# Kernel tuning notes

Hardware: AMD Instinct MI355X
Metric: run time of the kernel (lower is better)

The kernel has to match this reference:

```python
import jax, jax.numpy as jnp
import numpy as np

N_NODES = 50000
N_EDGES = 600000
D = 128
LN_EPS = 1e-5


def setup_inputs() -> dict:
    key = jax.random.key(0)
    ks = jax.random.split(key, 10)
    s = 1.0 / np.sqrt(D)
    return {
        "node_reps": jax.random.normal(ks[0], (N_NODES, D), jnp.float32),
        "edge_reps": jax.random.normal(ks[1], (N_EDGES, D), jnp.float32),
        "src_idx": jax.random.randint(ks[2], (N_EDGES,), 0, N_NODES, jnp.int32),
        "dst_idx": jnp.sort(jax.random.randint(ks[3], (N_EDGES,), 0, N_NODES, jnp.int32)),
        "Wq": jax.random.normal(ks[4], (D, D), jnp.float32) * s,
        "Wk": jax.random.normal(ks[5], (D, D), jnp.float32) * s,
        "Wv": jax.random.normal(ks[6], (D, D), jnp.float32) * s,
        "Wo": jax.random.normal(ks[7], (D, D), jnp.float32) * s,
        "ln_gamma": jnp.ones((D,), jnp.float32),
        "ln_beta": jnp.zeros((D,), jnp.float32),
        "W1": jax.random.normal(ks[8], (3 * D, D), jnp.float32) * (1.0 / np.sqrt(3 * D)),
        "b1": jnp.zeros((D,), jnp.float32),
        "W2": jax.random.normal(ks[9], (D, D), jnp.float32) * s,
        "b2": jnp.zeros((D,), jnp.float32),
    }


def _layer_norm(x, g, b):
    mu = jnp.mean(x, axis=-1, keepdims=True)
    var = jnp.mean(jnp.square(x - mu), axis=-1, keepdims=True)
    return (x - mu) * jax.lax.rsqrt(var + LN_EPS) * g + b


def reference(node_reps, edge_reps, src_idx, dst_idx, Wq, Wk, Wv, Wo,
              ln_gamma, ln_beta, W1, b1, W2, b2):
    n_nodes, d = node_reps.shape
    # dense projections once per node (kernel-friendly GEMMs)
    q = node_reps @ Wq                                  # [N, d]
    k_nodes = node_reps @ Wk                            # [N, d]
    v_nodes = node_reps @ Wv                            # [N, d]
    # per-edge gather + edge bias
    k_e = k_nodes[src_idx] + edge_reps                  # [E, d]
    scores = jnp.sum(q[dst_idx] * k_e, axis=-1) / jnp.sqrt(jnp.float32(d))  # [E]
    # segment softmax over edges sharing the same dst node
    seg_max = jax.ops.segment_max(scores, dst_idx, num_segments=n_nodes)
    ex = jnp.exp(scores - seg_max[dst_idx])
    denom = jax.ops.segment_sum(ex, dst_idx, num_segments=n_nodes)
    alpha = ex / denom[dst_idx]                          # [E]
    v_e = v_nodes[src_idx] + edge_reps                   # [E, d]
    agg = jax.ops.segment_sum(alpha[:, None] * v_e, dst_idx, num_segments=n_nodes)  # [N, d]
    updated = _layer_norm(node_reps + agg @ Wo, ln_gamma, ln_beta)  # [N, d]
    # triplet fusion MLP over (dst node, edge, src node)
    h_trip = jnp.concatenate([node_reps[dst_idx], edge_reps, node_reps[src_idx]], axis=-1)  # [E, 3d]
    fused = jax.nn.relu(h_trip @ W1 + b1) @ W2 + b2      # [E, d]
    return updated, fused
```

## Files before the change

### kernel.cpp

```cpp
#include <hip/hip_runtime.h>
#include <hip/hip_bf16.h>

#define NN 50000
#define NE 600000
#define D 128

typedef __bf16 bf16x8 __attribute__((ext_vector_type(8)));
typedef __bf16 bf16x4 __attribute__((ext_vector_type(4)));
typedef float f32x4 __attribute__((ext_vector_type(4)));


static __device__ __forceinline__ void gload_lds16(const void* g, void* l) {
  __builtin_amdgcn_global_load_lds(
      (const __attribute__((address_space(1))) unsigned int*)g,
      (__attribute__((address_space(3))) unsigned int*)l, 16, 0, 0);
}

static __device__ __forceinline__ bf16x8 load_a_frag_nc(const float* __restrict__ A,
                                                        int row, int k0) {
  const f32x4* p = (const f32x4*)(A + (size_t)row * D + k0);
  f32x4 v0 = p[0], v1 = p[1];
  bf16x8 r;
  r[0] = (__bf16)v0[0]; r[1] = (__bf16)v0[1]; r[2] = (__bf16)v0[2]; r[3] = (__bf16)v0[3];
  r[4] = (__bf16)v1[0]; r[5] = (__bf16)v1[1]; r[6] = (__bf16)v1[2]; r[7] = (__bf16)v1[3];
  return r;
}

static __device__ __forceinline__ void stage_a_tile64(const float* __restrict__ A, int M,
                                                      int row_base, char* lds, int tid) {
  const int l32 = tid & 31;
  const int g = tid >> 5;
#pragma unroll
  for (int it = 0; it < 8; ++it) {
    int rl = it * 8 + g;
    int r = row_base + rl;
    f32x4 v = {};
    if (r < M) v = *(const f32x4*)(A + (size_t)r * D + l32 * 4);
    bf16x4 b;
    b[0] = (__bf16)v[0]; b[1] = (__bf16)v[1]; b[2] = (__bf16)v[2]; b[3] = (__bf16)v[3];
    int byte = (rl * 256 + l32 * 8) ^ ((rl & 7) << 4);
    *(bf16x4*)(lds + byte) = b;
  }
}

static __device__ __forceinline__ bf16x8 read_a_frag(const char* lds, int rl, int k0) {
  int byte = (rl * 256 + k0 * 2) ^ ((rl & 7) << 4);
  return *(const bf16x8*)(lds + byte);
}

template <int CTRL>
static __device__ __forceinline__ float dpp_add(float x) {
  int v = __builtin_amdgcn_update_dpp(0, __float_as_int(x), CTRL, 0xf, 0xf, true);
  return x + __int_as_float(v);
}

static __device__ __forceinline__ float red32(float x) {
  x = dpp_add<0xB1>(x);
  x = dpp_add<0x4E>(x);
  x = dpp_add<0x124>(x);
  x = dpp_add<0x128>(x);
  return x + __shfl_xor(x, 16, 64);
}

struct PrepArgs {
  const float* W[8];
  __bf16* WT[8];
  const int* dst;
  int* offs;
};

__global__ void prep_all(PrepArgs pa) {
  int b = blockIdx.x;
  if (b < 512) {
    int w = b >> 6;
    int t = (b & 63) * 256 + threadIdx.x;
    int n = t & 127, k = t >> 7;
    pa.WT[w][n * 128 + k] = (__bf16)pa.W[w][k * 128 + n];
  } else {
    int n = (b - 512) * 256 + threadIdx.x;
    if (n > NN) return;
    int lo = 0, hi = NE;
    while (lo < hi) {
      int mid = (lo + hi) >> 1;
      if (pa.dst[mid] < n) lo = mid + 1; else hi = mid;
    }
    pa.offs[n] = lo;
  }
}

struct GemmBatch {
  const __bf16* BT[5];
  void* C[5];
  const float* bias[5];
  int mode[5];
};

__global__ __launch_bounds__(256) void gemm_k128_b(const float* __restrict__ A,
                                                   GemmBatch gb, int M) {
  __shared__ __align__(16) char atile[64 * 256];
  const int tid = threadIdx.x;
  const int lane = tid & 63;
  const int wave = tid >> 6;
  const int wr = wave >> 1, wc = wave & 1;
  const int row0 = blockIdx.x * 64;
  const int col0 = wc * 64;
  const int lr = lane & 15;
  const int lk = (lane >> 4) << 3;
  const int rr = (lane >> 4) * 4;

  stage_a_tile64(A, M, row0, atile, tid);
  __syncthreads();

#pragma unroll
  for (int y = 0; y < 5; ++y) {
    const __bf16* __restrict__ BT = gb.BT[y];
    f32x4 acc[2][4] = {};
#pragma unroll
    for (int kk = 0; kk < 4; ++kk) {
      const int k0 = kk * 32 + lk;
      bf16x8 a[2], b[4];
#pragma unroll
      for (int m = 0; m < 2; ++m) a[m] = read_a_frag(atile, wr * 32 + m * 16 + lr, k0);
#pragma unroll
      for (int n = 0; n < 4; ++n) b[n] = *(const bf16x8*)(BT + (size_t)(col0 + n * 16 + lr) * D + k0);
#pragma unroll
      for (int m = 0; m < 2; ++m)
#pragma unroll
        for (int n = 0; n < 4; ++n)
          acc[m][n] = __builtin_amdgcn_mfma_f32_16x16x32_bf16(a[m], b[n], acc[m][n], 0, 0, 0);
    }
    float bv[4] = {0.f, 0.f, 0.f, 0.f};
    if (gb.bias[y]) {
#pragma unroll
      for (int n = 0; n < 4; ++n) bv[n] = gb.bias[y][col0 + n * 16 + lr];
    }
    const int mode = gb.mode[y];
#pragma unroll
    for (int m = 0; m < 2; ++m)
#pragma unroll
      for (int j = 0; j < 4; ++j) {
        const int r = row0 + wr * 32 + m * 16 + rr + j;
        if (r < M) {
#pragma unroll
          for (int n = 0; n < 4; ++n) {
            const int c = col0 + n * 16 + lr;
            const float val = acc[m][n][j] + bv[n];
            if (mode == 0) {
              ((float*)gb.C[y])[(size_t)r * D + c] = val;
            } else if (mode == 1) {
              ((__bf16*)gb.C[y])[(size_t)r * D + c] = (__bf16)val;
            } else if (mode == 2) {
              ((__bf16*)gb.C[y])[(size_t)r * 256 + c] = (__bf16)val;
            } else {
              ((__bf16*)gb.C[y])[(size_t)r * 256 + 128 + c] = (__bf16)val;
            }
          }
        }
      }
  }
}

#define LD1(P, K, J, SV)                                                     \
  do {                                                                       \
    const int jj_ = (J);                                                     \
    const int jc_ = jj_ < jm ? jj_ : 0;                                      \
    int si_ = __shfl((SV), jj_ & 31, 32);                                    \
    si_ = jj_ < jm ? si_ : 0;                                                \
    kb##P[K] = *(const bf16x4*)(KV + (size_t)si_ * 256 + (l32 << 2));        \
    vb##P[K] = *(const bf16x4*)(KV + (size_t)si_ * 256 + 128 + (l32 << 2));  \
    eb##P[K] = *(const f32x4*)(edge + (size_t)(s0 + jc_) * D + (l32 << 2));  \
  } while (0)

#define LOADC(P, C)                                                          \
  do {                                                                       \
    const int c4_ = (C) * 4;                                                 \
    const int sv_ = (c4_ < 32) ? sidx0 : sidx1;                              \
    LD1(P, 0, c4_ + 0, sv_); LD1(P, 1, c4_ + 1, sv_);                        \
    LD1(P, 2, c4_ + 2, sv_); LD1(P, 3, c4_ + 3, sv_);                        \
  } while (0)

#define CP1(P, K, J)                                                         \
  do {                                                                       \
    const int jj_ = (J);                                                     \
    f32x4 ef_ = eb##P[K];                                                    \
    float x0_ = (float)kb##P[K][0] + ef_[0];                                 \
    float x1_ = (float)kb##P[K][1] + ef_[1];                                 \
    float x2_ = (float)kb##P[K][2] + ef_[2];                                 \
    float x3_ = (float)kb##P[K][3] + ef_[3];                                 \
    float pp_ = fmaf(qs[1], x1_, qs[0] * x0_) + fmaf(qs[3], x3_, qs[2] * x2_); \
    float s_ = red32(pp_);                                                   \
    float w_ = jj_ < jm ? exp2f(s_) : 0.f;                                   \
    l += w_;                                                                 \
    a[0] = fmaf(w_, (float)vb##P[K][0] + ef_[0], a[0]);                      \
    a[1] = fmaf(w_, (float)vb##P[K][1] + ef_[1], a[1]);                      \
    a[2] = fmaf(w_, (float)vb##P[K][2] + ef_[2], a[2]);                      \
    a[3] = fmaf(w_, (float)vb##P[K][3] + ef_[3], a[3]);                      \
  } while (0)

#define COMPC(P, C)                                                          \
  do {                                                                       \
    const int cc4_ = (C) * 4;                                                \
    CP1(P, 0, cc4_ + 0); CP1(P, 1, cc4_ + 1);                                \
    CP1(P, 2, cc4_ + 2); CP1(P, 3, cc4_ + 3);                                \
  } while (0)

__global__ __launch_bounds__(256) __attribute__((amdgpu_waves_per_eu(3)))
void fused_edge_attn(
    const float* __restrict__ edge,
    const __bf16* __restrict__ W1bT,
    const __bf16* __restrict__ W2T,
    const __bf16* __restrict__ P1,
    const __bf16* __restrict__ P3,
    const int* __restrict__ dst,
    const int* __restrict__ src,
    const float* __restrict__ b2,
    float* __restrict__ out_fused,
    const float* __restrict__ Q,
    const __bf16* __restrict__ KV,
    const int* __restrict__ offs,
    const __bf16* __restrict__ WoT,
    const float* __restrict__ noderep,
    const float* __restrict__ gamma,
    const float* __restrict__ beta,
    float* __restrict__ out_updated) {
  __shared__ __align__(16) char bufA[64 * 256];
  __shared__ __align__(16) char bufB[64 * 256];
  const int tid = threadIdx.x;
  const int grp = blockIdx.x / 5;
  const int role = blockIdx.x % 5;

  if (role >= 2) {
    const int ebi = grp * 3 + (role - 2);
    const int eb = ebi * 64;
    const int lane = tid & 63;
    const int wave = tid >> 6;
    const int wr = wave >> 1, wc = wave & 1;
    const int lr = lane & 15;
    const int lk = (lane >> 4) << 3;
    const int col0 = wc * 64;

    {
      const int gr = lane >> 4;
      const int slot = lane & 15;
      int di[4], sg[4];
#pragma unroll
      for (int c = 0; c < 4; ++c) {
        int rl = wave * 16 + c * 4 + gr;
        di[c] = dst[eb + rl];
        sg[c] = src[eb + rl];
      }
#pragma unroll
      for (int c = 0; c < 4; ++c) {
        int rl = wave * 16 + c * 4 + gr;
        int sb = (slot * 16) ^ ((rl & 7) << 4);
        gload_lds16((const char*)(P1 + (size_t)di[c] * D) + sb,
                    bufA + (wave * 16 + c * 4) * 256);
        gload_lds16((const char*)(P3 + (size_t)sg[c] * D) + sb,
                    bufB + (wave * 16 + c * 4) * 256);
      }
    }

    f32x4 acc[2][4] = {};
#pragma unroll
    for (int kk = 0; kk < 4; ++kk) {
      const int k0 = kk * 32 + lk;
      bf16x8 a[2], b[4];
#pragma unroll
      for (int m = 0; m < 2; ++m) a[m] = load_a_frag_nc(edge, eb + wr * 32 + m * 16 + lr, k0);
#pragma unroll
      for (int n = 0; n < 4; ++n) b[n] = *(const bf16x8*)(W1bT + (size_t)(col0 + n * 16 + lr) * D + k0);
#pragma unroll
      for (int m = 0; m < 2; ++m)
#pragma unroll
        for (int n = 0; n < 4; ++n)
          acc[m][n] = __builtin_amdgcn_mfma_f32_16x16x32_bf16(a[m], b[n], acc[m][n], 0, 0, 0);
    }
    __syncthreads();

    const int rr = (lane >> 4) * 4;
#pragma unroll
    for (int m = 0; m < 2; ++m) {
#pragma unroll
      for (int j = 0; j < 4; ++j) {
        int rl = wr * 32 + m * 16 + rr + j;
#pragma unroll
        for (int n = 0; n < 4; ++n) {
          int c = col0 + n * 16 + lr;
          int byte = (rl * 256 + c * 2) ^ ((rl & 7) << 4);
          float g1 = (float)*(const __bf16*)(bufA + byte);
          float g3 = (float)*(const __bf16*)(bufB + byte);
          float v = fmaxf(acc[m][n][j] + g1 + g3, 0.f);
          *(__bf16*)(bufA + byte) = (__bf16)v;
        }
      }
    }
    __syncthreads();

    float b2v[4];
#pragma unroll
    for (int n = 0; n < 4; ++n) b2v[n] = b2[col0 + n * 16 + lr];
    f32x4 acc2[2][4] = {};
#pragma unroll
    for (int kk = 0; kk < 4; ++kk) {
      const int k0 = kk * 32 + lk;
      bf16x8 a[2], b[4];
#pragma unroll
      for (int m = 0; m < 2; ++m) a[m] = read_a_frag(bufA, wr * 32 + m * 16 + lr, k0);
#pragma unroll
      for (int n = 0; n < 4; ++n) b[n] = *(const bf16x8*)(W2T + (size_t)(col0 + n * 16 + lr) * D + k0);
#pragma unroll
      for (int m = 0; m < 2; ++m)
#pragma unroll
        for (int n = 0; n < 4; ++n)
          acc2[m][n] = __builtin_amdgcn_mfma_f32_16x16x32_bf16(a[m], b[n], acc2[m][n], 0, 0, 0);
    }
#pragma unroll
    for (int m = 0; m < 2; ++m)
#pragma unroll
      for (int j = 0; j < 4; ++j) {
        int rl = wr * 32 + m * 16 + rr + j;
        int e = eb + rl;
#pragma unroll
        for (int n = 0; n < 4; ++n) {
          int c = col0 + n * 16 + lr;
          out_fused[(size_t)e * D + c] = acc2[m][n][j] + b2v[n];
        }
      }
  } else {
    const int nw = tid >> 5;
    const int node = (grp * 2 + role) * 8 + nw;
    const int l32 = tid & 31;
    int s0 = offs[node], s1 = offs[node + 1];
    int cnt = s1 - s0;
    f32x4 q = *(const f32x4*)(Q + (size_t)node * D + l32 * 4);
    f32x4 qs;
    qs[0] = q[0] * 0.12751744f; qs[1] = q[1] * 0.12751744f;
    qs[2] = q[2] * 0.12751744f; qs[3] = q[3] * 0.12751744f;
    float l = 0.f;
    f32x4 a = {0.f, 0.f, 0.f, 0.f};

    const int jm = cnt < 64 ? cnt : 64;
    if (jm > 0) {
      int sidx0 = 0, sidx1 = 0;
      if (l32 < cnt) sidx0 = src[s0 + l32];
      if (l32 + 32 < cnt) sidx1 = src[s0 + 32 + l32];
      bf16x4 kb0[4], vb0[4]; f32x4 eb0[4];
      bf16x4 kb1[4], vb1[4]; f32x4 eb1[4];
      const int nch = (jm + 3) >> 2;
      LOADC(0, 0);
      for (int c = 0; c < nch; c += 2) {
        if (c + 1 < nch) LOADC(1, c + 1);
        COMPC(0, c);
        if (c + 2 < nch) LOADC(0, c + 2);
        if (c + 1 < nch) COMPC(1, c + 1);
      }
      for (int i = 64; i < cnt; ++i) {
        int si = src[s0 + i];
        bf16x4 kbx = *(const bf16x4*)(KV + (size_t)si * 256 + (l32 << 2));
        bf16x4 vbx = *(const bf16x4*)(KV + (size_t)si * 256 + 128 + (l32 << 2));
        f32x4 ef = *(const f32x4*)(edge + (size_t)(s0 + i) * D + (l32 << 2));
        float x0 = (float)kbx[0] + ef[0], x1 = (float)kbx[1] + ef[1];
        float x2 = (float)kbx[2] + ef[2], x3 = (float)kbx[3] + ef[3];
        float pp = fmaf(qs[1], x1, qs[0] * x0) + fmaf(qs[3], x3, qs[2] * x2);
        float w = exp2f(red32(pp));
        l += w;
        a[0] = fmaf(w, (float)vbx[0] + ef[0], a[0]);
        a[1] = fmaf(w, (float)vbx[1] + ef[1], a[1]);
        a[2] = fmaf(w, (float)vbx[2] + ef[2], a[2]);
        a[3] = fmaf(w, (float)vbx[3] + ef[3], a[3]);
      }
    }
    float inv = l > 0.f ? 1.f / l : 0.f;
    f32x4 r;
    r[0] = a[0] * inv; r[1] = a[1] * inv; r[2] = a[2] * inv; r[3] = a[3] * inv;

    {
      bf16x4 rb;
      rb[0] = (__bf16)r[0]; rb[1] = (__bf16)r[1];
      rb[2] = (__bf16)r[2]; rb[3] = (__bf16)r[3];
      int byte = (nw * 256 + l32 * 8) ^ ((nw & 7) << 4);
      *(bf16x4*)(bufA + byte) = rb;
    }
    __syncthreads();

    {
      const int wave = tid >> 6;
      const int lane = tid & 63;
      const int lr = lane & 15;
      const int lk = (lane >> 4) << 3;
      f32x4 acc[2] = {};
#pragma unroll
      for (int kk = 0; kk < 4; ++kk) {
        int k0 = kk * 32 + lk;
        bf16x8 af = read_a_frag(bufA, lr, k0);
#pragma unroll
        for (int t = 0; t < 2; ++t) {
          int n = wave * 2 + t;
          bf16x8 b = *(const bf16x8*)(WoT + (size_t)(n * 16 + lr) * D + k0);
          acc[t] = __builtin_amdgcn_mfma_f32_16x16x32_bf16(af, b, acc[t], 0, 0, 0);
        }
      }
      float* xl = (float*)bufB;
      const int rr = (lane >> 4) * 4;
      if (rr < 8) {
#pragma unroll
        for (int t = 0; t < 2; ++t) {
          int n = wave * 2 + t;
#pragma unroll
          for (int j = 0; j < 4; ++j)
            xl[(rr + j) * 128 + n * 16 + lr] = acc[t][j];
        }
      }
    }
    __syncthreads();

    {
      const float* xl = (const float*)bufB;
      f32x4 xv = *(const f32x4*)(xl + nw * 128 + l32 * 4);
      f32x4 nv = *(const f32x4*)(noderep + (size_t)node * D + l32 * 4);
      float x0 = xv[0] + nv[0], x1 = xv[1] + nv[1];
      float x2 = xv[2] + nv[2], x3 = xv[3] + nv[3];
      float s = red32(x0 + x1 + x2 + x3);
      float mu = s * (1.f / 128.f);
      float d0 = x0 - mu, d1 = x1 - mu, d2 = x2 - mu, d3 = x3 - mu;
      float vv = red32(d0 * d0 + d1 * d1 + d2 * d2 + d3 * d3);
      float rstd = rsqrtf(vv * (1.f / 128.f) + 1e-5f);
      f32x4 g = *(const f32x4*)(gamma + l32 * 4);
      f32x4 bb = *(const f32x4*)(beta + l32 * 4);
      f32x4 o;
      o[0] = d0 * rstd * g[0] + bb[0];
      o[1] = d1 * rstd * g[1] + bb[1];
      o[2] = d2 * rstd * g[2] + bb[2];
      o[3] = d3 * rstd * g[3] + bb[3];
      *(f32x4*)(out_updated + (size_t)node * D + l32 * 4) = o;
    }
  }
}

extern "C" void kernel_launch(void* const* d_in, const int* in_sizes, int n_in,
                              void* d_out, int out_size, void* d_ws, size_t ws_size,
                              hipStream_t stream) {
  const float* node = (const float*)d_in[0];
  const float* edge = (const float*)d_in[1];
  const int* src = (const int*)d_in[2];
  const int* dst = (const int*)d_in[3];
  const float* Wq = (const float*)d_in[4];
  const float* Wk = (const float*)d_in[5];
  const float* Wv = (const float*)d_in[6];
  const float* Wo = (const float*)d_in[7];
  const float* gamma = (const float*)d_in[8];
  const float* beta = (const float*)d_in[9];
  const float* W1 = (const float*)d_in[10];
  const float* b1 = (const float*)d_in[11];
  const float* W2 = (const float*)d_in[12];
  const float* b2 = (const float*)d_in[13];

  float* out_updated = (float*)d_out;
  float* out_fused = (float*)d_out + (size_t)NN * D;

  char* ws = (char*)d_ws;
  size_t o = 0;
  auto take = [&](size_t bytes) {
    char* p = ws + o;
    o = (o + bytes + 255) & ~(size_t)255;
    return p;
  };
  int* offs = (int*)take((NN + 1) * sizeof(int));
  __bf16* WqT = (__bf16*)take(128 * 128 * 2);
  __bf16* WkT = (__bf16*)take(128 * 128 * 2);
  __bf16* WvT = (__bf16*)take(128 * 128 * 2);
  __bf16* WoT = (__bf16*)take(128 * 128 * 2);
  __bf16* W1aT = (__bf16*)take(128 * 128 * 2);
  __bf16* W1bT = (__bf16*)take(128 * 128 * 2);
  __bf16* W1cT = (__bf16*)take(128 * 128 * 2);
  __bf16* W2T = (__bf16*)take(128 * 128 * 2);
  float* Qb = (float*)take((size_t)NN * D * 4);
  __bf16* KVb = (__bf16*)take((size_t)NN * 256 * 2);
  __bf16* P1b = (__bf16*)take((size_t)NN * D * 2);
  __bf16* P3b = (__bf16*)take((size_t)NN * D * 2);

  PrepArgs pa;
  pa.W[0] = Wq; pa.WT[0] = WqT;
  pa.W[1] = Wk; pa.WT[1] = WkT;
  pa.W[2] = Wv; pa.WT[2] = WvT;
  pa.W[3] = Wo; pa.WT[3] = WoT;
  pa.W[4] = W1; pa.WT[4] = W1aT;
  pa.W[5] = W1 + 128 * 128; pa.WT[5] = W1bT;
  pa.W[6] = W1 + 256 * 128; pa.WT[6] = W1cT;
  pa.W[7] = W2; pa.WT[7] = W2T;
  pa.dst = dst; pa.offs = offs;
  prep_all<<<512 + (NN + 256) / 256, 256, 0, stream>>>(pa);

  GemmBatch gb;
  gb.BT[0] = WqT;  gb.C[0] = Qb;  gb.bias[0] = nullptr; gb.mode[0] = 0;
  gb.BT[1] = WkT;  gb.C[1] = KVb; gb.bias[1] = nullptr; gb.mode[1] = 2;
  gb.BT[2] = WvT;  gb.C[2] = KVb; gb.bias[2] = nullptr; gb.mode[2] = 3;
  gb.BT[3] = W1aT; gb.C[3] = P1b; gb.bias[3] = b1;      gb.mode[3] = 1;
  gb.BT[4] = W1cT; gb.C[4] = P3b; gb.bias[4] = nullptr; gb.mode[4] = 1;
  gemm_k128_b<<<(NN + 63) / 64, 256, 0, stream>>>(node, gb, NN);

  fused_edge_attn<<<15625, 256, 0, stream>>>(edge, W1bT, W2T, P1b, P3b, dst, src,
                                             b2, out_fused, Qb, KVb, offs,
                                             WoT, node, gamma, beta, out_updated);
}
```

Measured before the change: 437.3 us.

## Balance attention edges across waves and split node GEMM over weight grid

Measured after the change: 437.7 us. Within noise of the previous version (+0.1%).

```diff
diff --git a/kernel.cpp b/kernel.cpp
--- a/kernel.cpp
+++ b/kernel.cpp
@@ -26,12 +26,12 @@
   return r;
 }
 
-static __device__ __forceinline__ void stage_a_tile64(const float* __restrict__ A, int M,
-                                                      int row_base, char* lds, int tid) {
+static __device__ __forceinline__ void stage_a_tile128(const float* __restrict__ A, int M,
+                                                       int row_base, char* lds, int tid) {
   const int l32 = tid & 31;
   const int g = tid >> 5;
 #pragma unroll
-  for (int it = 0; it < 8; ++it) {
+  for (int it = 0; it < 16; ++it) {
     int rl = it * 8 + g;
     int r = row_base + rl;
     f32x4 v = {};
@@ -97,99 +97,104 @@
 
 __global__ __launch_bounds__(256) void gemm_k128_b(const float* __restrict__ A,
                                                    GemmBatch gb, int M) {
-  __shared__ __align__(16) char atile[64 * 256];
+  __shared__ __align__(16) char atile[128 * 256];
+  const int y = blockIdx.y;
+  const __bf16* __restrict__ BT = gb.BT[y];
   const int tid = threadIdx.x;
   const int lane = tid & 63;
   const int wave = tid >> 6;
   const int wr = wave >> 1, wc = wave & 1;
-  const int row0 = blockIdx.x * 64;
+  const int row0 = blockIdx.x * 128;
   const int col0 = wc * 64;
   const int lr = lane & 15;
   const int lk = (lane >> 4) << 3;
+
+  stage_a_tile128(A, M, row0, atile, tid);
+  __syncthreads();
+
+  f32x4 acc[4][4] = {};
+#pragma unroll
+  for (int kk = 0; kk < 4; ++kk) {
+    const int k0 = kk * 32 + lk;
+    bf16x8 a[4], b[4];
+#pragma unroll
+    for (int m = 0; m < 4; ++m) a[m] = read_a_frag(atile, wr * 64 + m * 16 + lr, k0);
+#pragma unroll
+    for (int n = 0; n < 4; ++n) b[n] = *(const bf16x8*)(BT + (size_t)(col0 + n * 16 + lr) * D + k0);
+#pragma unroll
+    for (int m = 0; m < 4; ++m)
+#pragma unroll
+      for (int n = 0; n < 4; ++n)
+        acc[m][n] = __builtin_amdgcn_mfma_f32_16x16x32_bf16(a[m], b[n], acc[m][n], 0, 0, 0);
+  }
   const int rr = (lane >> 4) * 4;
-
-  stage_a_tile64(A, M, row0, atile, tid);
-  __syncthreads();
-
-#pragma unroll
-  for (int y = 0; y < 5; ++y) {
-    const __bf16* __restrict__ BT = gb.BT[y];
-    f32x4 acc[2][4] = {};
-#pragma unroll
-    for (int kk = 0; kk < 4; ++kk) {
-      const int k0 = kk * 32 + lk;
-      bf16x8 a[2], b[4];
-#pragma unroll
-      for (int m = 0; m < 2; ++m) a[m] = read_a_frag(atile, wr * 32 + m * 16 + lr, k0);
-#pragma unroll
-      for (int n = 0; n < 4; ++n) b[n] = *(const bf16x8*)(BT + (size_t)(col0 + n * 16 + lr) * D + k0);
-#pragma unroll
-      for (int m = 0; m < 2; ++m)
-#pragma unroll
-        for (int n = 0; n < 4; ++n)
-          acc[m][n] = __builtin_amdgcn_mfma_f32_16x16x32_bf16(a[m], b[n], acc[m][n], 0, 0, 0);
-    }
-    float bv[4] = {0.f, 0.f, 0.f, 0.f};
-    if (gb.bias[y]) {
-#pragma unroll
-      for (int n = 0; n < 4; ++n) bv[n] = gb.bias[y][col0 + n * 16 + lr];
-    }
-    const int mode = gb.mode[y];
-#pragma unroll
-    for (int m = 0; m < 2; ++m)
-#pragma unroll
-      for (int j = 0; j < 4; ++j) {
-        const int r = row0 + wr * 32 + m * 16 + rr + j;
-        if (r < M) {
-#pragma unroll
-          for (int n = 0; n < 4; ++n) {
-            const int c = col0 + n * 16 + lr;
-            const float val = acc[m][n][j] + bv[n];
-            if (mode == 0) {
-              ((float*)gb.C[y])[(size_t)r * D + c] = val;
-            } else if (mode == 1) {
-              ((__bf16*)gb.C[y])[(size_t)r * D + c] = (__bf16)val;
-            } else if (mode == 2) {
-              ((__bf16*)gb.C[y])[(size_t)r * 256 + c] = (__bf16)val;
-            } else {
-              ((__bf16*)gb.C[y])[(size_t)r * 256 + 128 + c] = (__bf16)val;
-            }
+  float bv[4] = {0.f, 0.f, 0.f, 0.f};
+  if (gb.bias[y]) {
+#pragma unroll
+    for (int n = 0; n < 4; ++n) bv[n] = gb.bias[y][col0 + n * 16 + lr];
+  }
+  const int mode = gb.mode[y];
+#pragma unroll
+  for (int m = 0; m < 4; ++m)
+#pragma unroll
+    for (int j = 0; j < 4; ++j) {
+      const int r = row0 + wr * 64 + m * 16 + rr + j;
+      if (r < M) {
+#pragma unroll
+        for (int n = 0; n < 4; ++n) {
+          const int c = col0 + n * 16 + lr;
+          const float val = acc[m][n][j] + bv[n];
+          if (mode == 0) {
+            ((float*)gb.C[y])[(size_t)r * D + c] = val;
+          } else if (mode == 1) {
+            ((__bf16*)gb.C[y])[(size_t)r * D + c] = (__bf16)val;
+          } else if (mode == 2) {
+            ((__bf16*)gb.C[y])[(size_t)r * 256 + c] = (__bf16)val;
+          } else {
+            ((__bf16*)gb.C[y])[(size_t)r * 256 + 128 + c] = (__bf16)val;
           }
         }
       }
-  }
-}
-
-#define LD1(P, K, J, SV)                                                     \
+    }
+}
+
+#define ALD1(P, K, JJ)                                                       \
   do {                                                                       \
-    const int jj_ = (J);                                                     \
-    const int jc_ = jj_ < jm ? jj_ : 0;                                      \
-    int si_ = __shfl((SV), jj_ & 31, 32);                                    \
-    si_ = jj_ < jm ? si_ : 0;                                                \
+    const int jj_ = (JJ);                                                    \
+    const int ok_ = jj_ < n32;                                               \
+    int si_ = __shfl(sidx, jj_ & 31, 32);                                    \
+    si_ = ok_ ? si_ : 0;                                                     \
+    const int ej_ = ok_ ? (myS + jj_) : myS;                                 \
     kb##P[K] = *(const bf16x4*)(KV + (size_t)si_ * 256 + (l32 << 2));        \
     vb##P[K] = *(const bf16x4*)(KV + (size_t)si_ * 256 + 128 + (l32 << 2));  \
-    eb##P[K] = *(const f32x4*)(edge + (size_t)(s0 + jc_) * D + (l32 << 2));  \
+    eb##P[K] = *(const f32x4*)(edge + (size_t)ej_ * D + (l32 << 2));         \
   } while (0)
 
-#define LOADC(P, C)                                                          \
+#define ALOADC(P, C)                                                         \
   do {                                                                       \
     const int c4_ = (C) * 4;                                                 \
-    const int sv_ = (c4_ < 32) ? sidx0 : sidx1;                              \
-    LD1(P, 0, c4_ + 0, sv_); LD1(P, 1, c4_ + 1, sv_);                        \
-    LD1(P, 2, c4_ + 2, sv_); LD1(P, 3, c4_ + 3, sv_);                        \
+    ALD1(P, 0, c4_ + 0); ALD1(P, 1, c4_ + 1);                                \
+    ALD1(P, 2, c4_ + 2); ALD1(P, 3, c4_ + 3);                                \
   } while (0)
 
-#define CP1(P, K, J)                                                         \
+#define ACP1(P, K, JJ)                                                       \
   do {                                                                       \
-    const int jj_ = (J);                                                     \
+    const int jj_ = (JJ);                                                    \
+    const int ok_ = jj_ < n32;                                               \
+    int dj_ = __shfl(didx, jj_ & 31, 32);                                    \
+    dj_ = ok_ ? dj_ : cur;                                                   \
+    if (dj_ != cur) {                                                        \
+      flush();                                                               \
+      cur = dj_;                                                             \
+      qs = *(const f32x4*)(qlds + ((cur - n0) << 7) + (l32 << 2));           \
+    }                                                                        \
     f32x4 ef_ = eb##P[K];                                                    \
     float x0_ = (float)kb##P[K][0] + ef_[0];                                 \
     float x1_ = (float)kb##P[K][1] + ef_[1];                                 \
     float x2_ = (float)kb##P[K][2] + ef_[2];                                 \
     float x3_ = (float)kb##P[K][3] + ef_[3];                                 \
     float pp_ = fmaf(qs[1], x1_, qs[0] * x0_) + fmaf(qs[3], x3_, qs[2] * x2_); \
-    float s_ = red32(pp_);                                                   \
-    float w_ = jj_ < jm ? exp2f(s_) : 0.f;                                   \
+    float w_ = ok_ ? exp2f(red32(pp_)) : 0.f;                                \
     l += w_;                                                                 \
     a[0] = fmaf(w_, (float)vb##P[K][0] + ef_[0], a[0]);                      \
     a[1] = fmaf(w_, (float)vb##P[K][1] + ef_[1], a[1]);                      \
@@ -197,12 +202,14 @@
     a[3] = fmaf(w_, (float)vb##P[K][3] + ef_[3], a[3]);                      \
   } while (0)
 
-#define COMPC(P, C)                                                          \
+#define ACOMPC(P, C)                                                         \
   do {                                                                       \
-    const int cc4_ = (C) * 4;                                                \
-    CP1(P, 0, cc4_ + 0); CP1(P, 1, cc4_ + 1);                                \
-    CP1(P, 2, cc4_ + 2); CP1(P, 3, cc4_ + 3);                                \
+    const int c4_ = (C) * 4;                                                 \
+    ACP1(P, 0, c4_ + 0); ACP1(P, 1, c4_ + 1);                                \
+    ACP1(P, 2, c4_ + 2); ACP1(P, 3, c4_ + 3);                                \
   } while (0)
+
+#define CATT 0.12751744612764933f
 
 __global__ __launch_bounds__(256) __attribute__((amdgpu_waves_per_eu(3)))
 void fused_edge_attn(
@@ -328,37 +335,71 @@
       }
   } else {
     const int nw = tid >> 5;
-    const int node = (grp * 2 + role) * 8 + nw;
     const int l32 = tid & 31;
-    int s0 = offs[node], s1 = offs[node + 1];
-    int cnt = s1 - s0;
-    f32x4 q = *(const f32x4*)(Q + (size_t)node * D + l32 * 4);
-    f32x4 qs;
-    qs[0] = q[0] * 0.12751744f; qs[1] = q[1] * 0.12751744f;
-    qs[2] = q[2] * 0.12751744f; qs[3] = q[3] * 0.12751744f;
-    float l = 0.f;
-    f32x4 a = {0.f, 0.f, 0.f, 0.f};
-
-    const int jm = cnt < 64 ? cnt : 64;
-    if (jm > 0) {
-      int sidx0 = 0, sidx1 = 0;
-      if (l32 < cnt) sidx0 = src[s0 + l32];
-      if (l32 + 32 < cnt) sidx1 = src[s0 + 32 + l32];
+    const int n0 = (grp * 2 + role) * 8;
+    float* qlds = (float*)bufA;
+    float* nodeAcc = (float*)bufB;
+
+    {
+      f32x4 qv = *(const f32x4*)(Q + (size_t)(n0 + nw) * D + (l32 << 2));
+      f32x4 qsc;
+      qsc[0] = qv[0] * CATT; qsc[1] = qv[1] * CATT;
+      qsc[2] = qv[2] * CATT; qsc[3] = qv[3] * CATT;
+      *(f32x4*)(qlds + nw * 128 + (l32 << 2)) = qsc;
+      for (int i = tid; i < 8 * 132; i += 256) nodeAcc[i] = 0.f;
+    }
+    __syncthreads();
+
+    const int e0 = offs[n0], e1 = offs[n0 + 8];
+    const int L = e1 - e0;
+    const int per = (L + 7) >> 3;
+    const int myS = e0 + nw * per;
+    const int myE = (myS + per < e1) ? (myS + per) : e1;
+    const int n = myE - myS;
+
+    if (n > 0) {
+      const int n32 = n < 32 ? n : 32;
+      int sidx = 0, didx = 0;
+      {
+        int gi = myS + l32;
+        if (l32 < n) { sidx = src[gi]; didx = dst[gi]; }
+      }
+      int cur = __shfl(didx, 0, 32);
+      f32x4 qs = *(const f32x4*)(qlds + ((cur - n0) << 7) + (l32 << 2));
+      float l = 0.f;
+      f32x4 a = {0.f, 0.f, 0.f, 0.f};
+      auto flush = [&]() {
+        float* na = nodeAcc + (cur - n0) * 132;
+        atomicAdd(na + (l32 << 2) + 0, a[0]);
+        atomicAdd(na + (l32 << 2) + 1, a[1]);
+        atomicAdd(na + (l32 << 2) + 2, a[2]);
+        atomicAdd(na + (l32 << 2) + 3, a[3]);
+        if (l32 == 0) atomicAdd(na + 128, l);
+        a[0] = 0.f; a[1] = 0.f; a[2] = 0.f; a[3] = 0.f;
+        l = 0.f;
+      };
+
       bf16x4 kb0[4], vb0[4]; f32x4 eb0[4];
       bf16x4 kb1[4], vb1[4]; f32x4 eb1[4];
-      const int nch = (jm + 3) >> 2;
-      LOADC(0, 0);
+      const int nch = (n32 + 3) >> 2;
+      ALOADC(0, 0);
       for (int c = 0; c < nch; c += 2) {
-        if (c + 1 < nch) LOADC(1, c + 1);
-        COMPC(0, c);
-        if (c + 2 < nch) LOADC(0, c + 2);
-        if (c + 1 < nch) COMPC(1, c + 1);
-      }
-      for (int i = 64; i < cnt; ++i) {
-        int si = src[s0 + i];
+        if (c + 1 < nch) ALOADC(1, c + 1);
+        ACOMPC(0, c);
+        if (c + 2 < nch) ALOADC(0, c + 2);
+        if (c + 1 < nch) ACOMPC(1, c + 1);
+      }
+      for (int i = myS + 32; i < myE; ++i) {
+        int si = src[i];
+        int dj = dst[i];
+        if (dj != cur) {
+          flush();
+          cur = dj;
+          qs = *(const f32x4*)(qlds + ((cur - n0) << 7) + (l32 << 2));
+        }
         bf16x4 kbx = *(const bf16x4*)(KV + (size_t)si * 256 + (l32 << 2));
         bf16x4 vbx = *(const bf16x4*)(KV + (size_t)si * 256 + 128 + (l32 << 2));
-        f32x4 ef = *(const f32x4*)(edge + (size_t)(s0 + i) * D + (l32 << 2));
+        f32x4 ef = *(const f32x4*)(edge + (size_t)i * D + (l32 << 2));
         float x0 = (float)kbx[0] + ef[0], x1 = (float)kbx[1] + ef[1];
         float x2 = (float)kbx[2] + ef[2], x3 = (float)kbx[3] + ef[3];
         float pp = fmaf(qs[1], x1, qs[0] * x0) + fmaf(qs[3], x3, qs[2] * x2);
@@ -369,15 +410,17 @@
         a[2] = fmaf(w, (float)vbx[2] + ef[2], a[2]);
         a[3] = fmaf(w, (float)vbx[3] + ef[3], a[3]);
       }
-    }
-    float inv = l > 0.f ? 1.f / l : 0.f;
-    f32x4 r;
-    r[0] = a[0] * inv; r[1] = a[1] * inv; r[2] = a[2] * inv; r[3] = a[3] * inv;
+      flush();
+    }
+    __syncthreads();
 
     {
+      float lsum = nodeAcc[nw * 132 + 128];
+      f32x4 av = *(const f32x4*)(nodeAcc + nw * 132 + (l32 << 2));
+      float inv = lsum > 0.f ? 1.f / lsum : 0.f;
       bf16x4 rb;
-      rb[0] = (__bf16)r[0]; rb[1] = (__bf16)r[1];
-      rb[2] = (__bf16)r[2]; rb[3] = (__bf16)r[3];
+      rb[0] = (__bf16)(av[0] * inv); rb[1] = (__bf16)(av[1] * inv);
+      rb[2] = (__bf16)(av[2] * inv); rb[3] = (__bf16)(av[3] * inv);
       int byte = (nw * 256 + l32 * 8) ^ ((nw & 7) << 4);
       *(bf16x4*)(bufA + byte) = rb;
     }
@@ -395,8 +438,8 @@
         bf16x8 af = read_a_frag(bufA, lr, k0);
 #pragma unroll
         for (int t = 0; t < 2; ++t) {
-          int n = wave * 2 + t;
-          bf16x8 b = *(const bf16x8*)(WoT + (size_t)(n * 16 + lr) * D + k0);
+          int nn = wave * 2 + t;
+          bf16x8 b = *(const bf16x8*)(WoT + (size_t)(nn * 16 + lr) * D + k0);
           acc[t] = __builtin_amdgcn_mfma_f32_16x16x32_bf16(af, b, acc[t], 0, 0, 0);
         }
       }
@@ -405,16 +448,17 @@
       if (rr < 8) {
 #pragma unroll
         for (int t = 0; t < 2; ++t) {
-          int n = wave * 2 + t;
+          int nn = wave * 2 + t;
 #pragma unroll
           for (int j = 0; j < 4; ++j)
-            xl[(rr + j) * 128 + n * 16 + lr] = acc[t][j];
+            xl[(rr + j) * 128 + nn * 16 + lr] = acc[t][j];
         }
       }
     }
     __syncthreads();
 
     {
+      const int node = n0 + nw;
       const float* xl = (const float*)bufB;
       f32x4 xv = *(const f32x4*)(xl + nw * 128 + l32 * 4);
       f32x4 nv = *(const f32x4*)(noderep + (size_t)node * D + l32 * 4);
@@ -491,13 +535,14 @@
   pa.dst = dst; pa.offs = offs;
   prep_all<<<512 + (NN + 256) / 256, 256, 0, stream>>>(pa);
 
+  int gnode = (NN + 127) / 128;
   GemmBatch gb;
   gb.BT[0] = WqT;  gb.C[0] = Qb;  gb.bias[0] = nullptr; gb.mode[0] = 0;
   gb.BT[1] = WkT;  gb.C[1] = KVb; gb.bias[1] = nullptr; gb.mode[1] = 2;
   gb.BT[2] = WvT;  gb.C[2] = KVb; gb.bias[2] = nullptr; gb.mode[2] = 3;
   gb.BT[3] = W1aT; gb.C[3] = P1b; gb.bias[3] = b1;      gb.mode[3] = 1;
   gb.BT[4] = W1cT; gb.C[4] = P3b; gb.bias[4] = nullptr; gb.mode[4] = 1;
-  gemm_k128_b<<<(NN + 63) / 64, 256, 0, stream>>>(node, gb, NN);
+  gemm_k128_b<<<dim3(gnode, 5), 256, 0, stream>>>(node, gb, NN);
 
   fused_edge_attn<<<15625, 256, 0, stream>>>(edge, W1bT, W2T, P1b, P3b, dst, src,
                                              b2, out_fused, Qb, KVb, offs,
```
